# Kernel tuning notes

Measured on AMD Instinct MI355X. Metric: run time of the kernel, lower is better.

Reference implementation:

```python
import jax, jax.numpy as jnp
import numpy as np

B, C, H, W = 16, 256, 32, 32
K = 3          # kernel size
KK = K * K     # matrix_batch = 9 kernel positions
N = 256        # out_channels = n (power of 2, nstack = 1)


def setup_inputs() -> dict:
    key = jax.random.key(0)
    k1, k2, k3, k4 = jax.random.split(key, 4)
    s = 1.0 / np.sqrt(2.0)  # repo's 'regular' param init scale
    return {
        "x": jax.random.normal(k1, (B, C, H, W), jnp.float32),
        "twiddle1": jax.random.normal(k2, (KK, N - 1, 2, 2), jnp.float32) * s,
        "twiddle2": jax.random.normal(k3, (KK, N - 1, 2, 2), jnp.float32) * s,
        "bias": jax.random.normal(k4, (KK, N), jnp.float32) * 0.01,
    }


def _butterfly_tied(twiddle, x, increasing):
    """Tied-weight butterfly multiply.
    twiddle: (s, n-1, 2, 2); x: (b, s, n). At stride st, twiddle[:, st-1:2*st-1]
    (length st) is shared across the n/(2*st) blocks (matches butterfly_mult_torch).
    """
    b, s, n = x.shape
    m = n.bit_length() - 1  # log2(n)
    strides = [1 << i for i in range(m)]
    if not increasing:
        strides = strides[::-1]
    for st in strides:
        t = twiddle[:, st - 1:2 * st - 1]            # (s, st, 2, 2)
        xr = x.reshape(b, s, n // (2 * st), 2, st)   # (b, s, g, 2, st)
        # out[b,s,g,i,l] = sum_k t[s,l,i,k] * xr[b,s,g,k,l]
        x = jnp.einsum('slik,bsgkl->bsgil', t, xr).reshape(b, s, n)
    return x


def reference(x, twiddle1, twiddle2, bias):
    b, c, h, w = x.shape
    # im2col / F.unfold with kernel 3, pad 1, stride 1 -> (b, c, 9, h*w),
    # kernel positions in row-major order (matches torch unfold layout).
    xp = jnp.pad(x, ((0, 0), (0, 0), (1, 1), (1, 1)))
    patches = jnp.stack(
        [xp[:, :, i:i + h, j:j + w] for i in range(K) for j in range(K)], axis=2
    )  # (b, c, 9, h, w)
    inp = patches.reshape(b, c, KK, h * w).transpose(0, 3, 2, 1)
    inp = inp.reshape(b * h * w, KK, c)  # (batch*h*w, 9, c)
    # BB^T: B^T (decreasing stride) then B (increasing stride), bias on last.
    y = _butterfly_tied(twiddle1, inp, increasing=False)
    y = _butterfly_tied(twiddle2, y, increasing=True) + bias  # bias: (9, N)
    out = y.mean(axis=1)  # average over the 9 kernel positions -> (b*h*w, N)
    return out.reshape(b, h * w, N).transpose(0, 2, 1).reshape(b, N, h, w)
```

## Files before the change

### kernel.cpp

```cpp
#include <hip/hip_runtime.h>
#include <hip/hip_bf16.h>

typedef __attribute__((ext_vector_type(8))) short short8;
typedef __attribute__((ext_vector_type(4))) float float4v;
typedef __attribute__((ext_vector_type(16))) float float16v;

#define XT_BYTES (16*32*34*34*8*2)
#define WG_BYTES (9*4*4*8*64*8*2)

__global__ __launch_bounds__(256) void k_prep(const float* __restrict__ x,
                                              const float* __restrict__ tw1,
                                              const float* __restrict__ tw2,
                                              const float* __restrict__ bias,
                                              __hip_bfloat16* __restrict__ xTg,
                                              __hip_bfloat16* __restrict__ Wg,
                                              float* __restrict__ biasout) {
  __shared__ __align__(16) char smem[256 * 33 * 4];
  int blk = blockIdx.x;
  int tid = threadIdx.x;

  if (blk < 512) {
    float* tile = (float*)smem;
    char* xTB = (char*)xTg;
    int h = blk & 31, b = blk >> 5;
    {
      int w4 = (tid & 7) * 4, c0 = tid >> 3;
#pragma unroll
      for (int j = 0; j < 8; ++j) {
        int ci = c0 + 32 * j;
        float4 v = *(const float4*)&x[((b * 256 + ci) * 32 + h) * 32 + w4];
        *(float4*)&tile[ci * 33 + w4] = v;
      }
    }
    __syncthreads();
    {
      int g0 = tid >> 5, w = tid & 31;
#pragma unroll
      for (int gi = 0; gi < 4; ++gi) {
        int g = gi * 8 + g0;
        union { short8 s; __hip_bfloat16 hv[8]; } pk;
#pragma unroll
        for (int cc = 0; cc < 8; ++cc)
          pk.hv[cc] = __float2bfloat16(tile[(g * 8 + cc) * 33 + w]);
        *(short8*)(xTB + ((((b * 32 + g) * 34 + h + 1) * 34) + (w + 1)) * 16) = pk.s;
      }
    }
    if (h < 2) {
      uint4 z4 = {0u, 0u, 0u, 0u};
      int edge = h * 33;
      for (int i = tid; i < 32 * 34; i += 256) {
        int g = i / 34, w = i - g * 34;
        *(uint4*)(xTB + ((((b * 32 + g) * 34 + edge) * 34) + w) * 16) = z4;
      }
      for (int i = tid; i < 32 * 32; i += 256) {
        int g = i >> 5, hh = 1 + (i & 31);
        *(uint4*)(xTB + ((((b * 32 + g) * 34 + hh) * 34) + edge) * 16) = z4;
      }
    }
    return;
  }

  int wblk = blk - 512;
  if (wblk == 144) {
    if (tid < 256) {
      float a = 0.f;
#pragma unroll
      for (int s = 0; s < 9; ++s) a += bias[s * 256 + tid];
      biasout[tid] = a * (1.f / 9.f);
    }
    return;
  }
  float* mat = (float*)smem;
  float* tws = (float*)(smem + 17408);
  int sidx = wblk >> 4;
  int colbase = (wblk & 15) * 16;

  for (int i = tid; i < 255 * 4; i += 256) {
    tws[i]           = tw1[sidx * 255 * 4 + i];
    tws[255 * 4 + i] = tw2[sidx * 255 * 4 + i];
  }
  {
    int r = tid;
#pragma unroll
    for (int c = 0; c < 16; ++c) mat[r * 17 + c] = (r == colbase + c) ? 1.f : 0.f;
  }

  int c  = tid & 15;
  int pg = tid >> 4;
  for (int ph = 0; ph < 2; ++ph) {
    for (int si = 0; si < 8; ++si) {
      int lg = ph ? si : (7 - si);
      int st = 1 << lg;
      __syncthreads();
      float x0[8], x1[8], t0[8], t1[8], t2[8], t3[8];
#pragma unroll
      for (int i = 0; i < 8; ++i) {
        int qp = pg * 8 + i;
        int li = qp & (st - 1);
        int gi = qp >> lg;
        int p0 = (gi << (lg + 1)) | li;
        int p1 = p0 + st;
        float4 tv = *(const float4*)&tws[(ph * 255 + st - 1 + li) * 4];
        t0[i] = tv.x; t1[i] = tv.y; t2[i] = tv.z; t3[i] = tv.w;
        x0[i] = mat[p0 * 17 + c];
        x1[i] = mat[p1 * 17 + c];
      }
#pragma unroll
      for (int i = 0; i < 8; ++i) {
        int qp = pg * 8 + i;
        int li = qp & (st - 1);
        int gi = qp >> lg;
        int p0 = (gi << (lg + 1)) | li;
        int p1 = p0 + st;
        mat[p0 * 17 + c] = t0[i] * x0[i] + t1[i] * x1[i];
        mat[p1 * 17 + c] = t2[i] * x0[i] + t3[i] * x1[i];
      }
    }
  }
  __syncthreads();

  for (int idx = tid; idx < 256 * 16; idx += 256) {
    int r = idx >> 4, cc = idx & 15;
    int cg = colbase + cc;
    int pr = cg >> 6, g = (cg >> 3) & 7, c8 = cg & 7;
    int nq = r >> 6, nl = r & 63;
    int o = ((((sidx * 4 + pr) * 4 + nq) * 8 + g) * 64 + nl) * 8 + c8;
    Wg[o] = __float2bfloat16(mat[r * 17 + cc] * (1.f / 9.f));
  }
}

__global__ __launch_bounds__(256, 2) void k_gemm(const __hip_bfloat16* __restrict__ xTg,
                                                 const __hip_bfloat16* __restrict__ Wg,
                                                 const float* __restrict__ biasout,
                                                 float* __restrict__ out) {
  __shared__ __align__(64) char lds[32768];
  const char* WgB = (const char*)Wg;
  const char* xTB = (const char*)xTg;

  int blk = blockIdx.x;
  int nq = blk & 3;
  int pt = (blk >> 2) & 7;
  int b  = blk >> 5;
  int h0 = pt * 4;

  int tid  = threadIdx.x;
  int lane = tid & 63;
  int wk   = tid >> 6;
  int half = lane >> 5;
  int l31  = lane & 31;

  float16v acc[2][4];
#pragma unroll
  for (int mt = 0; mt < 2; ++mt)
#pragma unroll
    for (int p2 = 0; p2 < 4; ++p2)
#pragma unroll
      for (int e = 0; e < 16; ++e) acc[mt][p2][e] = 0.f;

  int aoff = ((2 * wk + half) * 64 + l31) * 16;
  int bbase = ((((b * 32 + 2 * wk + half) * 34 + h0) * 34) + l31) * 16;

#pragma unroll 2
  for (int p = 0; p < 4; ++p) {
    const char* Bp = xTB + bbase + p * (8 * 34 * 34) * 16;
    const char* Ap = WgB + (p * 4 + nq) * 8192;
#pragma unroll
    for (int si = 0; si < 3; ++si) {
#pragma unroll
      for (int sj = 0; sj < 3; ++sj) {
        const char* Aslab = Ap + (si * 3 + sj) * (16 * 8192);
        short8 a0 = *(const short8*)(Aslab + aoff);
        short8 a1 = *(const short8*)(Aslab + aoff + 32 * 16);
        const char* Bq = Bp + (si * 34 + sj) * 16;
        short8 b0 = *(const short8*)(Bq);
        short8 b1 = *(const short8*)(Bq + 34 * 16);
        short8 b2 = *(const short8*)(Bq + 68 * 16);
        short8 b3 = *(const short8*)(Bq + 102 * 16);
        acc[0][0] = __builtin_amdgcn_mfma_f32_32x32x16_bf16(a0, b0, acc[0][0], 0, 0, 0);
        acc[0][1] = __builtin_amdgcn_mfma_f32_32x32x16_bf16(a0, b1, acc[0][1], 0, 0, 0);
        acc[0][2] = __builtin_amdgcn_mfma_f32_32x32x16_bf16(a0, b2, acc[0][2], 0, 0, 0);
        acc[0][3] = __builtin_amdgcn_mfma_f32_32x32x16_bf16(a0, b3, acc[0][3], 0, 0, 0);
        acc[1][0] = __builtin_amdgcn_mfma_f32_32x32x16_bf16(a1, b0, acc[1][0], 0, 0, 0);
        acc[1][1] = __builtin_amdgcn_mfma_f32_32x32x16_bf16(a1, b1, acc[1][1], 0, 0, 0);
        acc[1][2] = __builtin_amdgcn_mfma_f32_32x32x16_bf16(a1, b2, acc[1][2], 0, 0, 0);
        acc[1][3] = __builtin_amdgcn_mfma_f32_32x32x16_bf16(a1, b3, acc[1][3], 0, 0, 0);
      }
    }
  }

  auto st16 = [&](int slot, const float16v& v) {
    char* base = lds + slot * 4096 + lane * 16;
    *(float4v*)(base)        = (float4v){v[0],  v[1],  v[2],  v[3]};
    *(float4v*)(base + 1024) = (float4v){v[4],  v[5],  v[6],  v[7]};
    *(float4v*)(base + 2048) = (float4v){v[8],  v[9],  v[10], v[11]};
    *(float4v*)(base + 3072) = (float4v){v[12], v[13], v[14], v[15]};
  };
  auto ld16add = [&](int slot, float16v& v) {
    const char* base = lds + slot * 4096 + lane * 16;
    float4v t0 = *(const float4v*)(base);
    float4v t1 = *(const float4v*)(base + 1024);
    float4v t2 = *(const float4v*)(base + 2048);
    float4v t3 = *(const float4v*)(base + 3072);
    v[0] += t0[0]; v[1] += t0[1]; v[2]  += t0[2]; v[3]  += t0[3];
    v[4] += t1[0]; v[5] += t1[1]; v[6]  += t1[2]; v[7]  += t1[3];
    v[8] += t2[0]; v[9] += t2[1]; v[10] += t2[2]; v[11] += t2[3];
    v[12] += t3[0]; v[13] += t3[1]; v[14] += t3[2]; v[15] += t3[3];
  };

  __syncthreads();
  if (wk >= 2) {
#pragma unroll
    for (int p2 = 0; p2 < 4; ++p2) st16((wk - 2) * 4 + p2, acc[0][p2]);
  }
  __syncthreads();
  if (wk < 2) {
#pragma unroll
    for (int p2 = 0; p2 < 4; ++p2) ld16add(wk * 4 + p2, acc[0][p2]);
  }
  __syncthreads();
  if (wk >= 2) {
#pragma unroll
    for (int p2 = 0; p2 < 4; ++p2) st16((wk - 2) * 4 + p2, acc[1][p2]);
  }
  __syncthreads();
  if (wk < 2) {
#pragma unroll
    for (int p2 = 0; p2 < 4; ++p2) ld16add(wk * 4 + p2, acc[1][p2]);
  }
  __syncthreads();
  if (wk == 1) {
#pragma unroll
    for (int p2 = 0; p2 < 4; ++p2) { st16(p2, acc[0][p2]); st16(4 + p2, acc[1][p2]); }
  }
  __syncthreads();
  if (wk == 0) {
#pragma unroll
    for (int p2 = 0; p2 < 4; ++p2) { ld16add(p2, acc[0][p2]); ld16add(4 + p2, acc[1][p2]); }
#pragma unroll
    for (int mt = 0; mt < 2; ++mt) {
#pragma unroll
      for (int reg = 0; reg < 16; ++reg) {
        int n = nq * 64 + mt * 32 + (reg & 3) + 8 * (reg >> 2) + 4 * half;
        float bv = biasout[n];
#pragma unroll
        for (int p2 = 0; p2 < 4; ++p2)
          out[((b * 256 + n) * 32 + h0 + p2) * 32 + l31] = acc[mt][p2][reg] + bv;
      }
    }
  }
}

extern "C" void kernel_launch(void* const* d_in, const int* in_sizes, int n_in,
                              void* d_out, int out_size, void* d_ws, size_t ws_size,
                              hipStream_t stream) {
  const float* x    = (const float*)d_in[0];
  const float* tw1  = (const float*)d_in[1];
  const float* tw2  = (const float*)d_in[2];
  const float* bias = (const float*)d_in[3];
  float* out = (float*)d_out;

  char* ws = (char*)d_ws;
  __hip_bfloat16* xTg = (__hip_bfloat16*)ws;
  __hip_bfloat16* Wg  = (__hip_bfloat16*)(ws + XT_BYTES);
  float* biasout      = (float*)(ws + XT_BYTES + WG_BYTES);

  k_prep<<<657, 256, 0, stream>>>(x, tw1, tw2, bias, xTg, Wg, biasout);
  k_gemm<<<512, 256, 0, stream>>>(xTg, Wg, biasout, out);
}
```

Measured before the change: 109.3 us.

## Software-pipeline GEMM main loop with async global-to-LDS weight staging ring

Replaces the plain unrolled loop in k_gemm with a hand-scheduled pipeline. Weight fragments are staged into a per-wave three-slot LDS ring using global_load_lds, and the activation loads for the next step are issued from registers while the current step's MFMAs run. Explicit vmcnt/lgkmcnt waits and sched barriers control the overlap. The aim is to hide global load latency behind MFMA work, at the cost of fragile hand-tuned wait counts and more register pressure.

```diff
diff --git a/kernel.cpp b/kernel.cpp
--- a/kernel.cpp
+++ b/kernel.cpp
@@ -129,11 +129,71 @@
   }
 }
 
+
+__device__ __forceinline__ void gload16(const char* g, char* l) {
+  __builtin_amdgcn_global_load_lds(
+      (const __attribute__((address_space(1))) void*)g,
+      (__attribute__((address_space(3))) void*)l, 16, 0, 0);
+}
+
+#define VMC4  asm volatile("s_waitcnt vmcnt(4)"  ::: "memory")
+#define VMC8  asm volatile("s_waitcnt vmcnt(8)"  ::: "memory")
+#define VMC10 asm volatile("s_waitcnt vmcnt(10)" ::: "memory")
+#define VMC12 asm volatile("s_waitcnt vmcnt(12)" ::: "memory")
+#define LGKM0 asm volatile("s_waitcnt lgkmcnt(0)" ::: "memory")
+#define SCHEDB __builtin_amdgcn_sched_barrier(0)
+
+#define STGA(GA, SLOT)                                                        \
+  { char* sd_ = ring + (SLOT) * 2048;                                         \
+    gload16((GA), sd_); gload16((GA) + 512, sd_ + 1024); }
+
+#define RD2(PAR, SLOT)                                                        \
+  { const char* sp_ = ring + (SLOT) * 2048 + lane * 16;                       \
+    rg[PAR][0] = *(const short8*)(sp_);                                       \
+    rg[PAR][1] = *(const short8*)(sp_ + 1024); }
+
+#define LDB4(PAR, GB)                                                         \
+  { const char* gb_ = (GB);                                                   \
+    rb[PAR][0] = *(const short8*)(gb_);                                       \
+    rb[PAR][1] = *(const short8*)(gb_ + 544);                                 \
+    rb[PAR][2] = *(const short8*)(gb_ + 1088);                                \
+    rb[PAR][3] = *(const short8*)(gb_ + 1632); }
+
+#define MFMA8(PAR)                                                            \
+  { acc[0][0] = __builtin_amdgcn_mfma_f32_32x32x16_bf16(rg[PAR][0], rb[PAR][0], acc[0][0], 0, 0, 0); \
+    acc[0][1] = __builtin_amdgcn_mfma_f32_32x32x16_bf16(rg[PAR][0], rb[PAR][1], acc[0][1], 0, 0, 0); \
+    acc[0][2] = __builtin_amdgcn_mfma_f32_32x32x16_bf16(rg[PAR][0], rb[PAR][2], acc[0][2], 0, 0, 0); \
+    acc[0][3] = __builtin_amdgcn_mfma_f32_32x32x16_bf16(rg[PAR][0], rb[PAR][3], acc[0][3], 0, 0, 0); \
+    acc[1][0] = __builtin_amdgcn_mfma_f32_32x32x16_bf16(rg[PAR][1], rb[PAR][0], acc[1][0], 0, 0, 0); \
+    acc[1][1] = __builtin_amdgcn_mfma_f32_32x32x16_bf16(rg[PAR][1], rb[PAR][1], acc[1][1], 0, 0, 0); \
+    acc[1][2] = __builtin_amdgcn_mfma_f32_32x32x16_bf16(rg[PAR][1], rb[PAR][2], acc[1][2], 0, 0, 0); \
+    acc[1][3] = __builtin_amdgcn_mfma_f32_32x32x16_bf16(rg[PAR][1], rb[PAR][3], acc[1][3], 0, 0, 0); }
+
+#define UBODY(K, PP)                                                          \
+  {                                                                           \
+    if ((K) == 0 && !(PP)) { VMC8; }                                          \
+    else if ((K) == 15 && (PP)) { VMC10; }                                    \
+    else if ((K) == 16 && (PP)) { VMC8; }                                     \
+    else if (!((K) == 17 && (PP))) { VMC12; }                                 \
+    if (!((K) == 17 && (PP))) {                                               \
+      RD2((((K) + 1) & 1), (((K) + 1) % 3));                                  \
+      LDB4((((K) + 1) & 1),                                                   \
+           gB0 + (((K) + 1) / 9) * 147968 + ((((K) + 1) % 9) / 3) * 544 +     \
+               ((((K) + 1) % 9) % 3) * 16);                                   \
+    }                                                                         \
+    MFMA8(((K) & 1));                                                         \
+    if (!((PP) && (K) >= 14)) {                                               \
+      LGKM0; SCHEDB;                                                          \
+      STGA(gA0 + (((K) + 4) / 9) * 32768 + (((K) + 4) % 9) * 131072,          \
+           (((K) + 1) % 3));                                                  \
+    }                                                                         \
+  }
+
 __global__ __launch_bounds__(256, 2) void k_gemm(const __hip_bfloat16* __restrict__ xTg,
                                                  const __hip_bfloat16* __restrict__ Wg,
                                                  const float* __restrict__ biasout,
                                                  float* __restrict__ out) {
-  __shared__ __align__(64) char lds[32768];
+  __shared__ __align__(128) char lds[32768];
   const char* WgB = (const char*)Wg;
   const char* xTB = (const char*)xTg;
 
@@ -157,35 +217,31 @@
 #pragma unroll
       for (int e = 0; e < 16; ++e) acc[mt][p2][e] = 0.f;
 
-  int aoff = ((2 * wk + half) * 64 + l31) * 16;
-  int bbase = ((((b * 32 + 2 * wk + half) * 34 + h0) * 34) + l31) * 16;
-
-#pragma unroll 2
-  for (int p = 0; p < 4; ++p) {
-    const char* Bp = xTB + bbase + p * (8 * 34 * 34) * 16;
-    const char* Ap = WgB + (p * 4 + nq) * 8192;
-#pragma unroll
-    for (int si = 0; si < 3; ++si) {
-#pragma unroll
-      for (int sj = 0; sj < 3; ++sj) {
-        const char* Aslab = Ap + (si * 3 + sj) * (16 * 8192);
-        short8 a0 = *(const short8*)(Aslab + aoff);
-        short8 a1 = *(const short8*)(Aslab + aoff + 32 * 16);
-        const char* Bq = Bp + (si * 34 + sj) * 16;
-        short8 b0 = *(const short8*)(Bq);
-        short8 b1 = *(const short8*)(Bq + 34 * 16);
-        short8 b2 = *(const short8*)(Bq + 68 * 16);
-        short8 b3 = *(const short8*)(Bq + 102 * 16);
-        acc[0][0] = __builtin_amdgcn_mfma_f32_32x32x16_bf16(a0, b0, acc[0][0], 0, 0, 0);
-        acc[0][1] = __builtin_amdgcn_mfma_f32_32x32x16_bf16(a0, b1, acc[0][1], 0, 0, 0);
-        acc[0][2] = __builtin_amdgcn_mfma_f32_32x32x16_bf16(a0, b2, acc[0][2], 0, 0, 0);
-        acc[0][3] = __builtin_amdgcn_mfma_f32_32x32x16_bf16(a0, b3, acc[0][3], 0, 0, 0);
-        acc[1][0] = __builtin_amdgcn_mfma_f32_32x32x16_bf16(a1, b0, acc[1][0], 0, 0, 0);
-        acc[1][1] = __builtin_amdgcn_mfma_f32_32x32x16_bf16(a1, b1, acc[1][1], 0, 0, 0);
-        acc[1][2] = __builtin_amdgcn_mfma_f32_32x32x16_bf16(a1, b2, acc[1][2], 0, 0, 0);
-        acc[1][3] = __builtin_amdgcn_mfma_f32_32x32x16_bf16(a1, b3, acc[1][3], 0, 0, 0);
-      }
-    }
+  const char* gAb = WgB + nq * 8192 + ((2 * wk + half) * 64 + l31) * 16;
+  const char* gBb = xTB + (((b * 32 + 2 * wk + half) * 34 + h0) * 34 + l31) * 16;
+
+  char* ring = lds + wk * 6144;
+
+  short8 rg[2][2];
+  short8 rb[2][4];
+
+  STGA(gAb, 0);
+  STGA(gAb + 131072, 1);
+  STGA(gAb + 262144, 2);
+  VMC4;
+  RD2(0, 0);
+  LDB4(0, gBb);
+  LGKM0; SCHEDB;
+  STGA(gAb + 3 * 131072, 0);
+
+  for (int p = 0; p <= 2; p += 2) {
+    const int pp = p;
+    const char* gA0 = gAb + p * 32768;
+    const char* gB0 = gBb + p * 147968;
+    UBODY(0, pp)  UBODY(1, pp)  UBODY(2, pp)  UBODY(3, pp)  UBODY(4, pp)
+    UBODY(5, pp)  UBODY(6, pp)  UBODY(7, pp)  UBODY(8, pp)  UBODY(9, pp)
+    UBODY(10, pp) UBODY(11, pp) UBODY(12, pp) UBODY(13, pp) UBODY(14, pp)
+    UBODY(15, pp) UBODY(16, pp) UBODY(17, pp)
   }
 
   auto st16 = [&](int slot, const float16v& v) {
```

New measurement: 109.4 us. No clear change (+0.1%).
